# Performance work log

Measured on AMD Instinct MI355X. Metric: run time of the kernel, lower is better.

Reference implementation:

```python
import jax, jax.numpy as jnp
import numpy as np

N = 50000          # num_nodes
E = 1600000        # num directed edges
IN_C = 128         # in_channels
OUT_C = 128        # out_channels
HEADS = 8
HFD = OUT_C // HEADS  # head_feat_dim = 16
NEG_SLOPE = 0.2


def setup_inputs() -> dict:
    key = jax.random.key(0)
    k1, k2, k3, k4, k5 = jax.random.split(key, 5)
    node_feats = jax.random.normal(k1, (N, IN_C), dtype=jnp.float32)
    edge_index = jax.random.randint(k2, (2, E), 0, N, dtype=jnp.int64)
    # parameters (xavier-ish scale, kept small so exp() stays in range)
    W = jax.random.normal(k3, (OUT_C, IN_C), dtype=jnp.float32) * (1.0 / np.sqrt(IN_C))
    a_left = jax.random.normal(k4, (HFD, HEADS), dtype=jnp.float32) * 0.1
    a_right = jax.random.normal(k5, (HFD, HEADS), dtype=jnp.float32) * 0.1
    bias = jnp.zeros((OUT_C,), dtype=jnp.float32)
    return {"node_feats": node_feats, "edge_index": edge_index,
            "W": W, "a_left": a_left, "a_right": a_right, "bias": bias}


def reference(node_feats, edge_index, W, a_left, a_right, bias):
    n = node_feats.shape[0]
    # embedding: Linear without bias, then split into heads -> [n, h, c]
    emb = (node_feats @ W.T).reshape(n, HEADS, HFD)
    # per-node attention logit halves: sum_c emb[n,h,c] * a[c,h] -> [n, h]
    left = jnp.einsum('nhc,ch->nh', emb, a_left)
    right = jnp.einsum('nhc,ch->nh', emb, a_right)
    src = edge_index[0]
    dst = edge_index[1]
    # edge logit: score(src, dst) uses a_left on src, a_right on dst
    e = left[src] + right[dst]                       # [E, h]
    e = jnp.where(e >= 0, e, NEG_SLOPE * e)          # leaky relu(0.2)
    w = jnp.exp(e)                                   # [E, h] (module uses raw exp)
    denom = jax.ops.segment_sum(w, dst, num_segments=n)  # [n, h]
    attn = w / denom[dst]                            # [E, h]
    msg = emb[src] * attn[:, :, None]                # [E, h, c]
    out = jax.ops.segment_sum(msg, dst, num_segments=n)  # [n, h, c]
    # concat heads + bias
    out = out.reshape(n, HEADS * HFD) + bias
    return out
```

## Files before the change

kernel.cpp:

```cpp
#include <hip/hip_runtime.h>
#include <hip/hip_bf16.h>

#define N_NODES 50000
#define N_EDGES 1600000
#define HEADS 8
#define HFD 16
#define CH 128

#define PART 128
#define NB 391
#define BCAP 5120
#define PA_T 512
#define PA_CHUNK 3200
#define PA_PER 7
#define PA_BLOCKS 500

#define QPART 32
#define QCAP 1536
#define AG_TASKS (NB * 4)
#define AG_BLOCKS 1568

typedef __bf16 bf16x8 __attribute__((ext_vector_type(8)));
typedef __bf16 bf16x4 __attribute__((ext_vector_type(4)));
typedef float f32x4 __attribute__((ext_vector_type(4)));

__device__ __forceinline__ float bf_lo(unsigned u) { return __uint_as_float(u << 16); }
__device__ __forceinline__ float bf_hi(unsigned u) { return __uint_as_float(u & 0xffff0000u); }

__global__ __launch_bounds__(256) void k_splitw(const float* __restrict__ W,
                                                const float* __restrict__ aL,
                                                const float* __restrict__ aR,
                                                __bf16* __restrict__ Whi,
                                                __bf16* __restrict__ Wlo,
                                                __bf16* __restrict__ Vhi,
                                                __bf16* __restrict__ Vlo,
                                                int* __restrict__ bucket_cnt) {
  int t = blockIdx.x * 256 + threadIdx.x;
  if (t < NB) bucket_cnt[t] = 0;
  if (t < CH * CH / 4) {
    f32x4 v = ((const f32x4*)W)[t];
    bf16x4 h, l;
#pragma unroll
    for (int i = 0; i < 4; ++i) {
      __bf16 hb = (__bf16)v[i];
      h[i] = hb;
      l[i] = (__bf16)(v[i] - (float)hb);
    }
    ((bf16x4*)Whi)[t] = h;
    ((bf16x4*)Wlo)[t] = l;
  }
  if (t < 16 * CH) {
    int j = t >> 7;
    int k = t & 127;
    int h = j & 7;
    const float* a = (j < 8) ? aL : aR;
    float v = 0.f;
#pragma unroll
    for (int c = 0; c < HFD; ++c) v += W[(h * HFD + c) * CH + k] * a[c * HEADS + h];
    __bf16 hb = (__bf16)v;
    Vhi[t] = hb;
    Vlo[t] = (__bf16)(v - (float)hb);
  }
}

__global__ __launch_bounds__(64) void k_emb(const float* __restrict__ X,
                                            const __bf16* __restrict__ Whi,
                                            const __bf16* __restrict__ Wlo,
                                            const __bf16* __restrict__ Vhi,
                                            const __bf16* __restrict__ Vlo,
                                            __bf16* __restrict__ embb,
                                            float* __restrict__ leftp,
                                            float* __restrict__ rightp) {
  int ntile = blockIdx.x;
  int lane = threadIdx.x;
  int c = lane & 15, quad = lane >> 4;
  const float* xp = X + (size_t)(ntile * 16 + c) * CH + quad * 8;
  bf16x8 xh[4], xl[4];
#pragma unroll
  for (int ks = 0; ks < 4; ++ks) {
    float4 x0 = *(const float4*)(xp + ks * 32);
    float4 x1 = *(const float4*)(xp + ks * 32 + 4);
    float xv[8] = {x0.x, x0.y, x0.z, x0.w, x1.x, x1.y, x1.z, x1.w};
#pragma unroll
    for (int j = 0; j < 8; ++j) {
      __bf16 hb = (__bf16)xv[j];
      xh[ks][j] = hb;
      xl[ks][j] = (__bf16)(xv[j] - (float)hb);
    }
  }
#pragma unroll
  for (int h = 0; h < HEADS; ++h) {
    const __bf16* wp = Whi + (size_t)(h * 16 + c) * CH + quad * 8;
    const __bf16* wlp = Wlo + (size_t)(h * 16 + c) * CH + quad * 8;
    f32x4 acc = {0.f, 0.f, 0.f, 0.f};
#pragma unroll
    for (int ks = 0; ks < 4; ++ks) {
      bf16x8 wh = *(const bf16x8*)(wp + ks * 32);
      bf16x8 wl = *(const bf16x8*)(wlp + ks * 32);
      acc = __builtin_amdgcn_mfma_f32_16x16x32_bf16(xl[ks], wh, acc, 0, 0, 0);
      acc = __builtin_amdgcn_mfma_f32_16x16x32_bf16(xh[ks], wl, acc, 0, 0, 0);
      acc = __builtin_amdgcn_mfma_f32_16x16x32_bf16(xh[ks], wh, acc, 0, 0, 0);
    }
#pragma unroll
    for (int r = 0; r < 4; ++r) {
      int node = ntile * 16 + quad * 4 + r;
      embb[(size_t)node * CH + h * HFD + c] = (__bf16)acc[r];
    }
  }
  {
    const __bf16* vp = Vhi + (size_t)c * CH + quad * 8;
    const __bf16* vlp = Vlo + (size_t)c * CH + quad * 8;
    f32x4 acc = {0.f, 0.f, 0.f, 0.f};
#pragma unroll
    for (int ks = 0; ks < 4; ++ks) {
      bf16x8 vh = *(const bf16x8*)(vp + ks * 32);
      bf16x8 vl = *(const bf16x8*)(vlp + ks * 32);
      acc = __builtin_amdgcn_mfma_f32_16x16x32_bf16(xl[ks], vh, acc, 0, 0, 0);
      acc = __builtin_amdgcn_mfma_f32_16x16x32_bf16(xh[ks], vl, acc, 0, 0, 0);
      acc = __builtin_amdgcn_mfma_f32_16x16x32_bf16(xh[ks], vh, acc, 0, 0, 0);
    }
#pragma unroll
    for (int r = 0; r < 4; ++r) {
      int node = ntile * 16 + quad * 4 + r;
      if (c < 8) leftp[node * HEADS + c] = acc[r];
      else rightp[node * HEADS + (c - 8)] = acc[r];
    }
  }
}

__global__ __launch_bounds__(PA_T) void k_bucket(const int* __restrict__ ei,
                                                 int* __restrict__ bucket_cnt,
                                                 unsigned* __restrict__ ebuf) {
  __shared__ unsigned sp[PA_CHUNK];
  __shared__ int hist[NB];
  __shared__ int lcur[NB];
  __shared__ int wbase[NB];
  __shared__ int scn[PA_T];
  int t = threadIdx.x;
  int base = blockIdx.x * PA_CHUNK;
  for (int i = t; i < NB; i += PA_T) hist[i] = 0;
  __syncthreads();
  unsigned pk[PA_PER];
#pragma unroll
  for (int i = 0; i < PA_PER; ++i) {
    int e = t + i * PA_T;
    pk[i] = 0xffffffffu;
    if (e < PA_CHUNK) {
      int src = ei[base + e];
      int dst = ei[N_EDGES + base + e];
      pk[i] = ((unsigned)(dst >> 7) << 23) | ((unsigned)(dst & 127) << 16) |
              (unsigned)src;
      atomicAdd(&hist[dst >> 7], 1);
    }
  }
  __syncthreads();
  scn[t] = (t < NB) ? hist[t] : 0;
  __syncthreads();
  int val = scn[t];
  for (int d = 1; d < PA_T; d <<= 1) {
    int o = (t >= d) ? scn[t - d] : 0;
    __syncthreads();
    val += o;
    scn[t] = val;
    __syncthreads();
  }
  if (t < NB) {
    int hv = hist[t];
    int lstart = val - hv;
    lcur[t] = lstart;
    int prior = hv ? atomicAdd(&bucket_cnt[t], hv) : 0;
    wbase[t] = t * BCAP + prior - lstart;
  }
  __syncthreads();
#pragma unroll
  for (int i = 0; i < PA_PER; ++i) {
    if (pk[i] != 0xffffffffu) {
      int b = pk[i] >> 23;
      int pos = atomicAdd(&lcur[b], 1);
      sp[pos] = pk[i];
    }
  }
  __syncthreads();
  for (int i = t; i < PA_CHUNK; i += PA_T) {
    unsigned p = sp[i];
    int b = p >> 23;
    int slot = wbase[b] + i;
    if (slot < (b + 1) * BCAP) ebuf[slot] = p;
  }
}

__global__ __launch_bounds__(256) void k_aggr(const int* __restrict__ bucket_cnt,
                                              const unsigned* __restrict__ ebuf,
                                              const __bf16* __restrict__ embb,
                                              const float* __restrict__ leftp,
                                              const float* __restrict__ rightp,
                                              const float* __restrict__ bias,
                                              float* __restrict__ out) {
  __shared__ unsigned short su[QCAP];
  __shared__ int hist[QPART];
  __shared__ int pfx[QPART];
  __shared__ int cur[QPART];
  int T = (blockIdx.x & 7) * (AG_BLOCKS / 8) + (blockIdx.x >> 3);
  if (T >= AG_TASKS) return;
  int b = T >> 2;
  int q = T & 3;
  int t = threadIdx.x;
  int cnt = bucket_cnt[b];
  if (cnt > BCAP) cnt = BCAP;
  int ebase = b * BCAP;
  if (t < QPART) hist[t] = 0;
  __syncthreads();
  for (int e4 = t * 4; e4 < cnt; e4 += 1024) {
    uint4 pp = *(const uint4*)(ebuf + ebase + e4);
    unsigned pj[4] = {pp.x, pp.y, pp.z, pp.w};
#pragma unroll
    for (int j = 0; j < 4; ++j) {
      if (e4 + j < cnt) {
        int dl = (pj[j] >> 16) & 127;
        if ((dl >> 5) == q) atomicAdd(&hist[dl & 31], 1);
      }
    }
  }
  __syncthreads();
  if (t < 64) {
    int v = (t < QPART) ? hist[t] : 0;
#pragma unroll
    for (int d = 1; d < QPART; d <<= 1) {
      int o = __shfl_up(v, d);
      if (t >= d) v += o;
    }
    if (t < QPART) {
      int ex = v - hist[t];
      pfx[t] = ex;
      cur[t] = ex;
    }
  }
  __syncthreads();
  for (int e4 = t * 4; e4 < cnt; e4 += 1024) {
    uint4 pp = *(const uint4*)(ebuf + ebase + e4);
    unsigned pj[4] = {pp.x, pp.y, pp.z, pp.w};
#pragma unroll
    for (int j = 0; j < 4; ++j) {
      if (e4 + j < cnt) {
        unsigned p = pj[j];
        int dl = (p >> 16) & 127;
        if ((dl >> 5) == q) {
          int pos = atomicAdd(&cur[dl & 31], 1);
          if (pos < QCAP) su[pos] = (unsigned short)(p & 0xffffu);
        }
      }
    }
  }
  __syncthreads();

  int wv = t >> 6;
  int lane = t & 63;
  int g = lane >> 4;
  int m = lane & 15;
  int h = m >> 1;
#pragma unroll 1
  for (int k = 0; k < 8; ++k) {
    int dl = wv * 8 + k;
    int dst = b * PART + q * QPART + dl;
    bool valid = dst < N_NODES;
    int beg = pfx[dl];
    int cd = hist[dl];
    if (beg + cd > QCAP) cd = QCAP - beg;
    float r = valid ? rightp[dst * HEADS + h] : 0.f;
    float acc[8] = {0.f, 0.f, 0.f, 0.f, 0.f, 0.f, 0.f, 0.f};
    float dsum = 0.f;
    if (cd > 0) {
      int sA0, sA1, sB0, sB1;
      uint4 uA0, uA1, uB0, uB1;
      float lA0, lA1, lB0, lB1;
#define STAGE(E0, s0, s1, u0, u1, l0, l1)                          \
      {                                                            \
        int i0 = (E0) + g, i1 = (E0) + 4 + g;                      \
        s0 = su[beg + ((i0 < cd) ? i0 : 0)];                       \
        s1 = su[beg + ((i1 < cd) ? i1 : 0)];                       \
        u0 = ((const uint4*)(embb + (size_t)s0 * CH))[m];          \
        u1 = ((const uint4*)(embb + (size_t)s1 * CH))[m];          \
        l0 = leftp[s0 * HEADS + h];                                \
        l1 = leftp[s1 * HEADS + h];                                \
      }
#define CONSUME(E0, u0, u1, l0, l1)                                \
      {                                                            \
        bool a0 = (E0) + g < cd, a1 = (E0) + 4 + g < cd;           \
        float x0 = l0 + r;                                         \
        x0 = (x0 >= 0.f) ? x0 : 0.2f * x0;                         \
        float w0 = a0 ? __expf(x0) : 0.f;                          \
        float x1 = l1 + r;                                         \
        x1 = (x1 >= 0.f) ? x1 : 0.2f * x1;                         \
        float w1 = a1 ? __expf(x1) : 0.f;                          \
        dsum += w0 + w1;                                           \
        acc[0] += w0 * bf_lo(u0.x) + w1 * bf_lo(u1.x);             \
        acc[1] += w0 * bf_hi(u0.x) + w1 * bf_hi(u1.x);             \
        acc[2] += w0 * bf_lo(u0.y) + w1 * bf_lo(u1.y);             \
        acc[3] += w0 * bf_hi(u0.y) + w1 * bf_hi(u1.y);             \
        acc[4] += w0 * bf_lo(u0.z) + w1 * bf_lo(u1.z);             \
        acc[5] += w0 * bf_hi(u0.z) + w1 * bf_hi(u1.z);             \
        acc[6] += w0 * bf_lo(u0.w) + w1 * bf_lo(u1.w);             \
        acc[7] += w0 * bf_hi(u0.w) + w1 * bf_hi(u1.w);             \
      }
      STAGE(0, sA0, sA1, uA0, uA1, lA0, lA1);
      int e0 = 0;
      while (true) {
        if (e0 + 8 < cd) STAGE(e0 + 8, sB0, sB1, uB0, uB1, lB0, lB1);
        CONSUME(e0, uA0, uA1, lA0, lA1);
        e0 += 8;
        if (e0 >= cd) break;
        if (e0 + 8 < cd) STAGE(e0 + 8, sA0, sA1, uA0, uA1, lA0, lA1);
        CONSUME(e0, uB0, uB1, lB0, lB1);
        e0 += 8;
        if (e0 >= cd) break;
      }
#undef STAGE
#undef CONSUME
    }
#pragma unroll
    for (int mask = 16; mask <= 32; mask <<= 1) {
      dsum += __shfl_xor(dsum, mask);
#pragma unroll
      for (int j = 0; j < 8; ++j) acc[j] += __shfl_xor(acc[j], mask);
    }
    if (g == 0 && valid) {
      float inv = (dsum > 0.f) ? 1.0f / dsum : 0.f;
      float4 b0 = ((const float4*)bias)[2 * m];
      float4 b1 = ((const float4*)bias)[2 * m + 1];
      float4 o0 = {acc[0] * inv + b0.x, acc[1] * inv + b0.y,
                   acc[2] * inv + b0.z, acc[3] * inv + b0.w};
      float4 o1 = {acc[4] * inv + b1.x, acc[5] * inv + b1.y,
                   acc[6] * inv + b1.z, acc[7] * inv + b1.w};
      ((float4*)(out + (size_t)dst * CH))[2 * m] = o0;
      ((float4*)(out + (size_t)dst * CH))[2 * m + 1] = o1;
    }
  }
}

extern "C" void kernel_launch(void* const* d_in, const int* in_sizes, int n_in,
                              void* d_out, int out_size, void* d_ws, size_t ws_size,
                              hipStream_t stream) {
  const float* X = (const float*)d_in[0];
  const int* ei = (const int*)d_in[1];
  const float* W = (const float*)d_in[2];
  const float* al = (const float*)d_in[3];
  const float* ar = (const float*)d_in[4];
  const float* bias = (const float*)d_in[5];
  float* out = (float*)d_out;

  unsigned* ebuf = (unsigned*)d_ws;
  __bf16* embb = (__bf16*)(ebuf + (size_t)NB * BCAP);
  __bf16* Whi = embb + (size_t)N_NODES * CH;
  __bf16* Wlo = Whi + CH * CH;
  __bf16* Vhi = Wlo + CH * CH;
  __bf16* Vlo = Vhi + 16 * CH;
  float* leftp = (float*)(Vlo + 16 * CH);
  float* rightp = leftp + (size_t)N_NODES * HEADS;
  int* bucket_cnt = (int*)(rightp + (size_t)N_NODES * HEADS);

  k_splitw<<<16, 256, 0, stream>>>(W, al, ar, Whi, Wlo, Vhi, Vlo, bucket_cnt);
  k_bucket<<<PA_BLOCKS, PA_T, 0, stream>>>(ei, bucket_cnt, ebuf);
  k_emb<<<N_NODES / 16, 64, 0, stream>>>(X, Whi, Wlo, Vhi, Vlo, embb, leftp, rightp);
  k_aggr<<<AG_BLOCKS, 256, 0, stream>>>(bucket_cnt, ebuf, embb, leftp, rightp, bias, out);
}
```

Measured before the change: 204.1 us.

## Interleave left logits into embedding rows and flatten per-wave edge pipeline

Packs each node's bf16 embedding together with its left attention logits into one 288-byte record, so the gather for a source node fetches both from a single row. The aggregation kernel is split into 8 sub-partitions of 16 destinations per bucket. This doubles the block count and shrinks the LDS edge list. Each wave now streams its 4 destinations' edges through one continuous software pipeline instead of restarting per destination, and right logits are preloaded into LDS. In exchange, every block rescans the whole bucket once more, and the padded row stride costs extra bytes per gather.

```diff
diff --git a/kernel.cpp b/kernel.cpp
--- a/kernel.cpp
+++ b/kernel.cpp
@@ -15,10 +15,13 @@
 #define PA_PER 7
 #define PA_BLOCKS 500
 
-#define QPART 32
-#define QCAP 1536
-#define AG_TASKS (NB * 4)
-#define AG_BLOCKS 1568
+#define OPART 16
+#define ECAP 896
+#define AG_TASKS (NB * 8)
+#define AG_CHUNK 392
+#define AG_BLOCKS 3136
+
+#define RSTRIDE_B 288
 
 typedef __bf16 bf16x8 __attribute__((ext_vector_type(8)));
 typedef __bf16 bf16x4 __attribute__((ext_vector_type(4)));
@@ -68,8 +71,7 @@
                                             const __bf16* __restrict__ Wlo,
                                             const __bf16* __restrict__ Vhi,
                                             const __bf16* __restrict__ Vlo,
-                                            __bf16* __restrict__ embb,
-                                            float* __restrict__ leftp,
+                                            unsigned char* __restrict__ embr,
                                             float* __restrict__ rightp) {
   int ntile = blockIdx.x;
   int lane = threadIdx.x;
@@ -104,7 +106,7 @@
 #pragma unroll
     for (int r = 0; r < 4; ++r) {
       int node = ntile * 16 + quad * 4 + r;
-      embb[(size_t)node * CH + h * HFD + c] = (__bf16)acc[r];
+      ((__bf16*)(embr + (size_t)node * RSTRIDE_B))[h * HFD + c] = (__bf16)acc[r];
     }
   }
   {
@@ -122,8 +124,10 @@
 #pragma unroll
     for (int r = 0; r < 4; ++r) {
       int node = ntile * 16 + quad * 4 + r;
-      if (c < 8) leftp[node * HEADS + c] = acc[r];
-      else rightp[node * HEADS + (c - 8)] = acc[r];
+      if (c < 8)
+        *(float*)(embr + (size_t)node * RSTRIDE_B + 256 + c * 4) = acc[r];
+      else
+        rightp[node * HEADS + (c - 8)] = acc[r];
     }
   }
 }
@@ -191,45 +195,50 @@
 
 __global__ __launch_bounds__(256) void k_aggr(const int* __restrict__ bucket_cnt,
                                               const unsigned* __restrict__ ebuf,
-                                              const __bf16* __restrict__ embb,
-                                              const float* __restrict__ leftp,
+                                              const unsigned char* __restrict__ embr,
                                               const float* __restrict__ rightp,
                                               const float* __restrict__ bias,
                                               float* __restrict__ out) {
-  __shared__ unsigned short su[QCAP];
-  __shared__ int hist[QPART];
-  __shared__ int pfx[QPART];
-  __shared__ int cur[QPART];
-  int T = (blockIdx.x & 7) * (AG_BLOCKS / 8) + (blockIdx.x >> 3);
+  __shared__ unsigned short su[ECAP];
+  __shared__ int hist[OPART];
+  __shared__ int pfx[OPART];
+  __shared__ int cur[OPART];
+  __shared__ float r_lds[OPART * HEADS];
+  int T = (blockIdx.x & 7) * AG_CHUNK + (blockIdx.x >> 3);
   if (T >= AG_TASKS) return;
-  int b = T >> 2;
-  int q = T & 3;
+  int b = T >> 3;
+  int oct = T & 7;
   int t = threadIdx.x;
+  int blockbase = b * PART + oct * OPART;
   int cnt = bucket_cnt[b];
   if (cnt > BCAP) cnt = BCAP;
   int ebase = b * BCAP;
-  if (t < QPART) hist[t] = 0;
+  if (t < OPART) hist[t] = 0;
+  if (t < OPART * HEADS) {
+    int dst = blockbase + (t >> 3);
+    r_lds[t] = (dst < N_NODES) ? rightp[dst * HEADS + (t & 7)] : 0.f;
+  }
   __syncthreads();
   for (int e4 = t * 4; e4 < cnt; e4 += 1024) {
     uint4 pp = *(const uint4*)(ebuf + ebase + e4);
     unsigned pj[4] = {pp.x, pp.y, pp.z, pp.w};
 #pragma unroll
-    for (int j = 0; j < 4; ++j) {
-      if (e4 + j < cnt) {
-        int dl = (pj[j] >> 16) & 127;
-        if ((dl >> 5) == q) atomicAdd(&hist[dl & 31], 1);
+    for (int jj = 0; jj < 4; ++jj) {
+      if (e4 + jj < cnt) {
+        int dl = (pj[jj] >> 16) & 127;
+        if ((dl >> 4) == oct) atomicAdd(&hist[dl & 15], 1);
       }
     }
   }
   __syncthreads();
   if (t < 64) {
-    int v = (t < QPART) ? hist[t] : 0;
-#pragma unroll
-    for (int d = 1; d < QPART; d <<= 1) {
+    int v = (t < OPART) ? hist[t] : 0;
+#pragma unroll
+    for (int d = 1; d < OPART; d <<= 1) {
       int o = __shfl_up(v, d);
       if (t >= d) v += o;
     }
-    if (t < QPART) {
+    if (t < OPART) {
       int ex = v - hist[t];
       pfx[t] = ex;
       cur[t] = ex;
@@ -240,13 +249,13 @@
     uint4 pp = *(const uint4*)(ebuf + ebase + e4);
     unsigned pj[4] = {pp.x, pp.y, pp.z, pp.w};
 #pragma unroll
-    for (int j = 0; j < 4; ++j) {
-      if (e4 + j < cnt) {
-        unsigned p = pj[j];
+    for (int jj = 0; jj < 4; ++jj) {
+      if (e4 + jj < cnt) {
+        unsigned p = pj[jj];
         int dl = (p >> 16) & 127;
-        if ((dl >> 5) == q) {
-          int pos = atomicAdd(&cur[dl & 31], 1);
-          if (pos < QCAP) su[pos] = (unsigned short)(p & 0xffffu);
+        if ((dl >> 4) == oct) {
+          int pos = atomicAdd(&cur[dl & 15], 1);
+          if (pos < ECAP) su[pos] = (unsigned short)(p & 0xffffu);
         }
       }
     }
@@ -258,81 +267,147 @@
   int g = lane >> 4;
   int m = lane & 15;
   int h = m >> 1;
-#pragma unroll 1
-  for (int k = 0; k < 8; ++k) {
-    int dl = wv * 8 + k;
-    int dst = b * PART + q * QPART + dl;
-    bool valid = dst < N_NODES;
-    int beg = pfx[dl];
-    int cd = hist[dl];
-    if (beg + cd > QCAP) cd = QCAP - beg;
-    float r = valid ? rightp[dst * HEADS + h] : 0.f;
-    float acc[8] = {0.f, 0.f, 0.f, 0.f, 0.f, 0.f, 0.f, 0.f};
-    float dsum = 0.f;
-    if (cd > 0) {
-      int sA0, sA1, sB0, sB1;
-      uint4 uA0, uA1, uB0, uB1;
-      float lA0, lA1, lB0, lB1;
-#define STAGE(E0, s0, s1, u0, u1, l0, l1)                          \
-      {                                                            \
-        int i0 = (E0) + g, i1 = (E0) + 4 + g;                      \
-        s0 = su[beg + ((i0 < cd) ? i0 : 0)];                       \
-        s1 = su[beg + ((i1 < cd) ? i1 : 0)];                       \
-        u0 = ((const uint4*)(embb + (size_t)s0 * CH))[m];          \
-        u1 = ((const uint4*)(embb + (size_t)s1 * CH))[m];          \
-        l0 = leftp[s0 * HEADS + h];                                \
-        l1 = leftp[s1 * HEADS + h];                                \
+  int wv4 = wv * 4;
+
+  auto cdcf = [&](int jl) -> int {
+    int p = pfx[jl], c = hist[jl], lim = ECAP - p;
+    return c < lim ? c : lim;
+  };
+
+  int ng = 0;
+#pragma unroll
+  for (int j = 0; j < 4; ++j) {
+    int c = cdcf(wv4 + j);
+    if (c > 0) ng += (c + 7) >> 3;
+  }
+
+  float acc0 = 0.f, acc1 = 0.f, acc2 = 0.f, acc3 = 0.f;
+  float acc4 = 0.f, acc5 = 0.f, acc6 = 0.f, acc7 = 0.f;
+  float dsum = 0.f, r = 0.f;
+  int jout = -1;
+
+  int sj = 0, se = 0;
+  while (sj < 4 && cdcf(wv4 + sj) <= 0) sj++;
+  int ks = 0, gi = 0, kc = 0;
+
+  int sA0 = 0, sA1 = 0, fA = 0, sB0 = 0, sB1 = 0, fB = 0;
+  uint4 uA0, uA1, uB0, uB1;
+  float lA0 = 0.f, lA1 = 0.f, lB0 = 0.f, lB1 = 0.f;
+  int gfA = 0, gfB = 0;
+
+#define SUF(S0v, S1v, Fv)                                                  \
+  {                                                                        \
+    int jl = wv4 + sj;                                                     \
+    int beg = pfx[jl];                                                     \
+    int cdc = cdcf(jl);                                                    \
+    int i0 = se + g, i1 = se + 4 + g;                                      \
+    int v0 = (i0 < cdc) ? 1 : 0, v1 = (i1 < cdc) ? 2 : 0;                  \
+    S0v = su[beg + (v0 ? i0 : 0)];                                         \
+    S1v = su[beg + (v1 ? i1 : 0)];                                         \
+    Fv = v0 | v1 | ((se == 0) ? 4 : 0);                                    \
+    se += 8;                                                               \
+    if (se >= cdc) {                                                       \
+      se = 0;                                                              \
+      do { sj++; } while (sj < 4 && cdcf(wv4 + sj) <= 0);                  \
+    }                                                                      \
+    ks++;                                                                  \
+  }
+
+#define GLI(U0, U1, L0, L1, GF, S0v, S1v, Fv)                              \
+  {                                                                        \
+    unsigned ro0 = (unsigned)S0v * RSTRIDE_B;                              \
+    unsigned ro1 = (unsigned)S1v * RSTRIDE_B;                              \
+    U0 = *(const uint4*)(embr + ro0 + m * 16);                             \
+    U1 = *(const uint4*)(embr + ro1 + m * 16);                             \
+    L0 = *(const float*)(embr + ro0 + 256 + h * 4);                        \
+    L1 = *(const float*)(embr + ro1 + 256 + h * 4);                        \
+    GF = Fv;                                                               \
+    gi++;                                                                  \
+  }
+
+#define FLUSH()                                                            \
+  {                                                                        \
+    float ds = dsum;                                                       \
+    ds += __shfl_xor(ds, 16); ds += __shfl_xor(ds, 32);                    \
+    float a0 = acc0 + __shfl_xor(acc0, 16);  a0 += __shfl_xor(a0, 32);     \
+    float a1 = acc1 + __shfl_xor(acc1, 16);  a1 += __shfl_xor(a1, 32);     \
+    float a2 = acc2 + __shfl_xor(acc2, 16);  a2 += __shfl_xor(a2, 32);     \
+    float a3 = acc3 + __shfl_xor(acc3, 16);  a3 += __shfl_xor(a3, 32);     \
+    float a4 = acc4 + __shfl_xor(acc4, 16);  a4 += __shfl_xor(a4, 32);     \
+    float a5 = acc5 + __shfl_xor(acc5, 16);  a5 += __shfl_xor(a5, 32);     \
+    float a6 = acc6 + __shfl_xor(acc6, 16);  a6 += __shfl_xor(a6, 32);     \
+    float a7 = acc7 + __shfl_xor(acc7, 16);  a7 += __shfl_xor(a7, 32);     \
+    int dsto = blockbase + wv4 + jout;                                     \
+    if (g == 0 && dsto < N_NODES) {                                        \
+      float inv = (ds > 0.f) ? 1.0f / ds : 0.f;                            \
+      float4 b0 = ((const float4*)bias)[2 * m];                            \
+      float4 b1 = ((const float4*)bias)[2 * m + 1];                        \
+      float4 o0 = {a0 * inv + b0.x, a1 * inv + b0.y,                       \
+                   a2 * inv + b0.z, a3 * inv + b0.w};                      \
+      float4 o1 = {a4 * inv + b1.x, a5 * inv + b1.y,                       \
+                   a6 * inv + b1.z, a7 * inv + b1.w};                      \
+      ((float4*)(out + (size_t)dsto * CH))[2 * m] = o0;                    \
+      ((float4*)(out + (size_t)dsto * CH))[2 * m + 1] = o1;                \
+    }                                                                      \
+  }
+
+#define CON(U0, U1, L0, L1, GF)                                            \
+  {                                                                        \
+    if (GF & 4) {                                                          \
+      if (jout >= 0) FLUSH();                                              \
+      jout++;                                                              \
+      while (jout < 3 && cdcf(wv4 + jout) <= 0) jout++;                    \
+      r = r_lds[(wv4 + jout) * 8 + h];                                     \
+      acc0 = acc1 = acc2 = acc3 = acc4 = acc5 = acc6 = acc7 = 0.f;         \
+      dsum = 0.f;                                                          \
+    }                                                                      \
+    float x0 = L0 + r; x0 = (x0 >= 0.f) ? x0 : 0.2f * x0;                  \
+    float w0 = (GF & 1) ? __expf(x0) : 0.f;                                \
+    float x1 = L1 + r; x1 = (x1 >= 0.f) ? x1 : 0.2f * x1;                  \
+    float w1 = (GF & 2) ? __expf(x1) : 0.f;                                \
+    dsum += w0 + w1;                                                       \
+    acc0 += w0 * bf_lo(U0.x) + w1 * bf_lo(U1.x);                           \
+    acc1 += w0 * bf_hi(U0.x) + w1 * bf_hi(U1.x);                           \
+    acc2 += w0 * bf_lo(U0.y) + w1 * bf_lo(U1.y);                           \
+    acc3 += w0 * bf_hi(U0.y) + w1 * bf_hi(U1.y);                           \
+    acc4 += w0 * bf_lo(U0.z) + w1 * bf_lo(U1.z);                           \
+    acc5 += w0 * bf_hi(U0.z) + w1 * bf_hi(U1.z);                           \
+    acc6 += w0 * bf_lo(U0.w) + w1 * bf_lo(U1.w);                           \
+    acc7 += w0 * bf_hi(U0.w) + w1 * bf_hi(U1.w);                           \
+    kc++;                                                                  \
+  }
+
+  if (ng > 0) {
+    SUF(sA0, sA1, fA);
+    if (ng > 1) SUF(sB0, sB1, fB);
+    GLI(uA0, uA1, lA0, lA1, gfA, sA0, sA1, fA);
+    while (true) {
+      if (gi < ng) GLI(uB0, uB1, lB0, lB1, gfB, sB0, sB1, fB);
+      if (ks < ng) SUF(sA0, sA1, fA);
+      CON(uA0, uA1, lA0, lA1, gfA);
+      if (kc >= ng) break;
+      if (gi < ng) GLI(uA0, uA1, lA0, lA1, gfA, sA0, sA1, fA);
+      if (ks < ng) SUF(sB0, sB1, fB);
+      CON(uB0, uB1, lB0, lB1, gfB);
+      if (kc >= ng) break;
+    }
+    FLUSH();
+  }
+#undef SUF
+#undef GLI
+#undef CON
+#undef FLUSH
+
+#pragma unroll
+  for (int j = 0; j < 4; ++j) {
+    if (cdcf(wv4 + j) <= 0) {
+      int dst = blockbase + wv4 + j;
+      if (g == 0 && dst < N_NODES) {
+        float4 b0 = ((const float4*)bias)[2 * m];
+        float4 b1 = ((const float4*)bias)[2 * m + 1];
+        ((float4*)(out + (size_t)dst * CH))[2 * m] = b0;
+        ((float4*)(out + (size_t)dst * CH))[2 * m + 1] = b1;
       }
-#define CONSUME(E0, u0, u1, l0, l1)                                \
-      {                                                            \
-        bool a0 = (E0) + g < cd, a1 = (E0) + 4 + g < cd;           \
-        float x0 = l0 + r;                                         \
-        x0 = (x0 >= 0.f) ? x0 : 0.2f * x0;                         \
-        float w0 = a0 ? __expf(x0) : 0.f;                          \
-        float x1 = l1 + r;                                         \
-        x1 = (x1 >= 0.f) ? x1 : 0.2f * x1;                         \
-        float w1 = a1 ? __expf(x1) : 0.f;                          \
-        dsum += w0 + w1;                                           \
-        acc[0] += w0 * bf_lo(u0.x) + w1 * bf_lo(u1.x);             \
-        acc[1] += w0 * bf_hi(u0.x) + w1 * bf_hi(u1.x);             \
-        acc[2] += w0 * bf_lo(u0.y) + w1 * bf_lo(u1.y);             \
-        acc[3] += w0 * bf_hi(u0.y) + w1 * bf_hi(u1.y);             \
-        acc[4] += w0 * bf_lo(u0.z) + w1 * bf_lo(u1.z);             \
-        acc[5] += w0 * bf_hi(u0.z) + w1 * bf_hi(u1.z);             \
-        acc[6] += w0 * bf_lo(u0.w) + w1 * bf_lo(u1.w);             \
-        acc[7] += w0 * bf_hi(u0.w) + w1 * bf_hi(u1.w);             \
-      }
-      STAGE(0, sA0, sA1, uA0, uA1, lA0, lA1);
-      int e0 = 0;
-      while (true) {
-        if (e0 + 8 < cd) STAGE(e0 + 8, sB0, sB1, uB0, uB1, lB0, lB1);
-        CONSUME(e0, uA0, uA1, lA0, lA1);
-        e0 += 8;
-        if (e0 >= cd) break;
-        if (e0 + 8 < cd) STAGE(e0 + 8, sA0, sA1, uA0, uA1, lA0, lA1);
-        CONSUME(e0, uB0, uB1, lB0, lB1);
-        e0 += 8;
-        if (e0 >= cd) break;
-      }
-#undef STAGE
-#undef CONSUME
-    }
-#pragma unroll
-    for (int mask = 16; mask <= 32; mask <<= 1) {
-      dsum += __shfl_xor(dsum, mask);
-#pragma unroll
-      for (int j = 0; j < 8; ++j) acc[j] += __shfl_xor(acc[j], mask);
-    }
-    if (g == 0 && valid) {
-      float inv = (dsum > 0.f) ? 1.0f / dsum : 0.f;
-      float4 b0 = ((const float4*)bias)[2 * m];
-      float4 b1 = ((const float4*)bias)[2 * m + 1];
-      float4 o0 = {acc[0] * inv + b0.x, acc[1] * inv + b0.y,
-                   acc[2] * inv + b0.z, acc[3] * inv + b0.w};
-      float4 o1 = {acc[4] * inv + b1.x, acc[5] * inv + b1.y,
-                   acc[6] * inv + b1.z, acc[7] * inv + b1.w};
-      ((float4*)(out + (size_t)dst * CH))[2 * m] = o0;
-      ((float4*)(out + (size_t)dst * CH))[2 * m + 1] = o1;
     }
   }
 }
@@ -349,17 +424,16 @@
   float* out = (float*)d_out;
 
   unsigned* ebuf = (unsigned*)d_ws;
-  __bf16* embb = (__bf16*)(ebuf + (size_t)NB * BCAP);
-  __bf16* Whi = embb + (size_t)N_NODES * CH;
+  unsigned char* embr = (unsigned char*)(ebuf + (size_t)NB * BCAP);
+  __bf16* Whi = (__bf16*)(embr + (size_t)N_NODES * RSTRIDE_B);
   __bf16* Wlo = Whi + CH * CH;
   __bf16* Vhi = Wlo + CH * CH;
   __bf16* Vlo = Vhi + 16 * CH;
-  float* leftp = (float*)(Vlo + 16 * CH);
-  float* rightp = leftp + (size_t)N_NODES * HEADS;
+  float* rightp = (float*)(Vlo + 16 * CH);
   int* bucket_cnt = (int*)(rightp + (size_t)N_NODES * HEADS);
 
   k_splitw<<<16, 256, 0, stream>>>(W, al, ar, Whi, Wlo, Vhi, Vlo, bucket_cnt);
   k_bucket<<<PA_BLOCKS, PA_T, 0, stream>>>(ei, bucket_cnt, ebuf);
-  k_emb<<<N_NODES / 16, 64, 0, stream>>>(X, Whi, Wlo, Vhi, Vlo, embb, leftp, rightp);
-  k_aggr<<<AG_BLOCKS, 256, 0, stream>>>(bucket_cnt, ebuf, embb, leftp, rightp, bias, out);
+  k_emb<<<N_NODES / 16, 64, 0, stream>>>(X, Whi, Wlo, Vhi, Vlo, embr, rightp);
+  k_aggr<<<AG_BLOCKS, 256, 0, stream>>>(bucket_cnt, ebuf, embr, rightp, bias, out);
 }
```

Measured after the change: 212.1 us. 3.9% more time.
